# Kernel tuning notes

Measured on AMD Instinct MI355X. Metric: run time of the kernel, lower is better.

## Reference

```python
import jax, jax.numpy as jnp
import numpy as np

NUM = 21  # classes 1..NUM scored; bin 0 is background, bin NUM+1 is a dump bin


def _class_counts(y_pred, y_true):
    # Single-pass histogram over all classes instead of O(num) full-tensor scans.
    yp = y_pred.ravel()
    yt = y_true.ravel()
    nbins = NUM + 2
    cnt_true = jnp.zeros((nbins,), jnp.float32).at[yt].add(1.0)
    cnt_pred = jnp.zeros((nbins,), jnp.float32).at[yp].add(1.0)
    # intersection: positions where pred == true, binned by label; mismatches -> dump bin
    inter_idx = jnp.where(yp == yt, yt, NUM + 1)
    inter = jnp.zeros((nbins,), jnp.float32).at[inter_idx].add(1.0)
    return cnt_true, cnt_pred, inter


def setup_inputs() -> dict:
    key = jax.random.key(0)
    k1, k2 = jax.random.split(key)
    shape = (32, 1024, 1024)
    y_pred = jax.random.randint(k1, shape, 0, NUM + 1, dtype=jnp.int32)
    y_true = jax.random.randint(k2, shape, 0, NUM + 1, dtype=jnp.int32)
    return {"y_pred": y_pred, "y_true": y_true}


def reference(y_pred, y_true):
    cnt_true, cnt_pred, inter = _class_counts(y_pred, y_true)
    # classes 1..NUM (label 0 skipped, as in the original loop over range(1, num+1))
    c_true = cnt_true[1:NUM + 1]
    c_pred = cnt_pred[1:NUM + 1]
    c_inter = inter[1:NUM + 1]
    union = c_true + c_pred - c_inter
    iou = (c_inter + 1e-6) / (union + 1e-6)  # [NUM]
    present = (c_true > 0).astype(jnp.float32)
    mIoU = jnp.sum(iou * present) / jnp.maximum(jnp.sum(present), 1.0)
    return mIoU, iou
```

## Files before the change

### kernel.cpp

```cpp
#include <hip/hip_runtime.h>


#define NUMC  21
#define NBINS 22
#define JBINS (NBINS * NBINS)
#define RSTR  485
#define NREP  4
#define GRID  2048
#define TPB   256

typedef int iv4 __attribute__((ext_vector_type(4)));

#define LDP(J) __builtin_nontemporal_load(yp4 + (J))
#define LDT(J) __builtin_nontemporal_load(yt4 + (J))
#define DS4(P, T)                                      \
    atomicAdd(&hh[(T).x * NBINS + (P).x], 1u);         \
    atomicAdd(&hh[(T).y * NBINS + (P).y], 1u);         \
    atomicAdd(&hh[(T).z * NBINS + (P).z], 1u);         \
    atomicAdd(&hh[(T).w * NBINS + (P).w], 1u);

__global__ void __launch_bounds__(256) hist_joint(
        const int* __restrict__ yp, const int* __restrict__ yt,
        unsigned int* __restrict__ partials, int n) {
    __shared__ unsigned int h[NREP * RSTR];
    for (int i = threadIdx.x; i < NREP * RSTR; i += TPB) h[i] = 0u;
    __syncthreads();

    const int lane = threadIdx.x & 63;
    const int wave = threadIdx.x >> 6;
    unsigned int* hh = h + wave * RSTR;

    const iv4* __restrict__ yp4 = (const iv4*)yp;
    const iv4* __restrict__ yt4 = (const iv4*)yt;
    const int n4 = n >> 2;

    const int gwave   = blockIdx.x * 4 + wave;
    const int nwaves  = GRID * 4;
    const int wstride = nwaves * 128;
    const int sweeps  = n4 / wstride;

    if (sweeps * wstride == n4 && (n & 3) == 0) {
        const int j0 = gwave * 128 + lane;
        iv4 pa = LDP(j0),      pb = LDP(j0 + 64);
        iv4 ta = LDT(j0),      tb = LDT(j0 + 64);
        for (int it = 1; it < sweeps; ++it) {
            const int j = j0 + it * wstride;
            iv4 npa = LDP(j),      npb = LDP(j + 64);
            iv4 nta = LDT(j),      ntb = LDT(j + 64);
            DS4(pa, ta) DS4(pb, tb)
            pa = npa; pb = npb; ta = nta; tb = ntb;
        }
        DS4(pa, ta) DS4(pb, tb)
    } else {
        const int stride = GRID * TPB;
        const int i0 = blockIdx.x * TPB + threadIdx.x;
        if (i0 < n4) {
            iv4 p = LDP(i0), t = LDT(i0);
            for (int j = i0 + stride; j < n4; j += stride) {
                iv4 pn = LDP(j), tn = LDT(j);
                DS4(p, t)
                p = pn; t = tn;
            }
            DS4(p, t)
        }
        if (blockIdx.x == 0 && threadIdx.x == 0) {
            for (int k = n4 << 2; k < n; k++)
                atomicAdd(&hh[yt[k] * NBINS + yp[k]], 1u);
        }
    }
#undef DS4
#undef LDP
#undef LDT

    __syncthreads();
    for (int c = threadIdx.x; c < JBINS; c += TPB) {
        unsigned int s = h[c] + h[RSTR + c] + h[2 * RSTR + c] + h[3 * RSTR + c];
        partials[(size_t)blockIdx.x * JBINS + c] = s;
    }
}

__global__ void __launch_bounds__(256) reduce_partials(
        const unsigned int* __restrict__ partials,
        unsigned int* __restrict__ g, int nblocks) {
    __shared__ unsigned int lds[256];
    const int c = blockIdx.x;
    unsigned int s = 0;
    for (int b = threadIdx.x; b < nblocks; b += 256)
        s += partials[(size_t)b * JBINS + c];
    lds[threadIdx.x] = s;
    __syncthreads();
    for (int w = 128; w > 0; w >>= 1) {
        if (threadIdx.x < w) lds[threadIdx.x] += lds[threadIdx.x + w];
        __syncthreads();
    }
    if (threadIdx.x == 0) g[c] = lds[0];
}

__global__ void finalize_kernel(const unsigned int* __restrict__ g,
                                float* __restrict__ out) {
    int lane = threadIdx.x;
    float iou = 0.0f, pres = 0.0f;
    if (lane >= 1 && lane <= NUMC) {
        unsigned int ct = 0, cp = 0;
        #pragma unroll
        for (int k = 0; k < NBINS; k++) {
            ct += g[lane * NBINS + k];
            cp += g[k * NBINS + lane];
        }
        unsigned int ci = g[lane * NBINS + lane];
        float u = (float)ct + (float)cp - (float)ci;
        iou = ((float)ci + 1e-6f) / (u + 1e-6f);
        pres = (ct > 0u) ? 1.0f : 0.0f;
        out[lane] = iou;
    }
    float v = iou * pres, pc = pres;
    #pragma unroll
    for (int off = 32; off > 0; off >>= 1) {
        v += __shfl_down(v, off);
        pc += __shfl_down(pc, off);
    }
    if (lane == 0) out[0] = v / fmaxf(pc, 1.0f);
}

extern "C" void kernel_launch(void* const* d_in, const int* in_sizes, int n_in,
                              void* d_out, int out_size, void* d_ws, size_t ws_size,
                              hipStream_t stream) {
    const int* yp = (const int*)d_in[0];
    const int* yt = (const int*)d_in[1];
    int n = in_sizes[0];
    float* out = (float*)d_out;

    unsigned int* g = (unsigned int*)d_ws;
    unsigned int* partials = g + JBINS;

    hist_joint<<<GRID, TPB, 0, stream>>>(yp, yt, partials, n);
    reduce_partials<<<JBINS, 256, 0, stream>>>(partials, g, GRID);
    finalize_kernel<<<1, 64, 0, stream>>>(g, out);
}
```

Baseline: 258.4 us.

## Fuse partial reduction and finalize into one kernel using a last-block ticket

Replaces the per-bin reduction kernel and the separate finalize kernel with one kernel. In it, 128 blocks each sum 16 rows of partial histograms, add the sums atomically into a global histogram, and the last block to arrive (found via an atomic ticket) computes the IoU output. The global histogram and the ticket are zeroed by block 0 of the histogram kernel. This drops one kernel launch and gives coalesced row reads in place of strided column reads, at the cost of global atomics and a fence-based handoff.

```diff
diff --git a/kernel.cpp b/kernel.cpp
--- a/kernel.cpp
+++ b/kernel.cpp
@@ -8,6 +8,8 @@
 #define NREP  4
 #define GRID  2048
 #define TPB   256
+#define RBLK  128
+#define ROWS  (GRID / RBLK)
 
 typedef int iv4 __attribute__((ext_vector_type(4)));
 
@@ -21,7 +23,13 @@
 
 __global__ void __launch_bounds__(256) hist_joint(
         const int* __restrict__ yp, const int* __restrict__ yt,
-        unsigned int* __restrict__ partials, int n) {
+        unsigned int* __restrict__ partials,
+        unsigned int* __restrict__ gz,
+        int n) {
+    if (blockIdx.x == 0) {
+        for (int i = threadIdx.x; i < JBINS + 8; i += TPB) gz[i] = 0u;
+    }
+
     __shared__ unsigned int h[NREP * RSTR];
     for (int i = threadIdx.x; i < NREP * RSTR; i += TPB) h[i] = 0u;
     __syncthreads();
@@ -79,35 +87,50 @@
     }
 }
 
-__global__ void __launch_bounds__(256) reduce_partials(
+__global__ void __launch_bounds__(256) reduce_finalize(
         const unsigned int* __restrict__ partials,
-        unsigned int* __restrict__ g, int nblocks) {
-    __shared__ unsigned int lds[256];
-    const int c = blockIdx.x;
-    unsigned int s = 0;
-    for (int b = threadIdx.x; b < nblocks; b += 256)
-        s += partials[(size_t)b * JBINS + c];
-    lds[threadIdx.x] = s;
+        unsigned int* __restrict__ g,
+        unsigned int* __restrict__ ticket,
+        float* __restrict__ out) {
+    const int tid = threadIdx.x;
+
+    unsigned int s0 = 0u, s1 = 0u;
+    const unsigned int* base = partials + (size_t)blockIdx.x * ROWS * JBINS;
+    #pragma unroll 4
+    for (int r = 0; r < ROWS; ++r) {
+        const unsigned int* row = base + (size_t)r * JBINS;
+        s0 += row[tid];
+        if (tid < JBINS - 256) s1 += row[tid + 256];
+    }
+    atomicAdd(&g[tid], s0);
+    if (tid < JBINS - 256) atomicAdd(&g[tid + 256], s1);
+
+    __shared__ unsigned int islast;
     __syncthreads();
-    for (int w = 128; w > 0; w >>= 1) {
-        if (threadIdx.x < w) lds[threadIdx.x] += lds[threadIdx.x + w];
-        __syncthreads();
+    if (tid == 0) {
+        __threadfence();
+        unsigned int old = __hip_atomic_fetch_add(
+            ticket, 1u, __ATOMIC_ACQ_REL, __HIP_MEMORY_SCOPE_AGENT);
+        islast = (old == RBLK - 1) ? 1u : 0u;
     }
-    if (threadIdx.x == 0) g[c] = lds[0];
-}
+    __syncthreads();
+    if (!islast) return;
+    __threadfence();
 
-__global__ void finalize_kernel(const unsigned int* __restrict__ g,
-                                float* __restrict__ out) {
-    int lane = threadIdx.x;
+    const int lane = tid;
+    if (lane >= 64) return;
     float iou = 0.0f, pres = 0.0f;
     if (lane >= 1 && lane <= NUMC) {
-        unsigned int ct = 0, cp = 0;
+        unsigned int ct = 0u, cp = 0u;
         #pragma unroll
         for (int k = 0; k < NBINS; k++) {
-            ct += g[lane * NBINS + k];
-            cp += g[k * NBINS + lane];
+            ct += __hip_atomic_load(&g[lane * NBINS + k],
+                                    __ATOMIC_RELAXED, __HIP_MEMORY_SCOPE_AGENT);
+            cp += __hip_atomic_load(&g[k * NBINS + lane],
+                                    __ATOMIC_RELAXED, __HIP_MEMORY_SCOPE_AGENT);
         }
-        unsigned int ci = g[lane * NBINS + lane];
+        unsigned int ci = __hip_atomic_load(&g[lane * NBINS + lane],
+                                    __ATOMIC_RELAXED, __HIP_MEMORY_SCOPE_AGENT);
         float u = (float)ct + (float)cp - (float)ci;
         iou = ((float)ci + 1e-6f) / (u + 1e-6f);
         pres = (ct > 0u) ? 1.0f : 0.0f;
@@ -131,9 +154,9 @@
     float* out = (float*)d_out;
 
     unsigned int* g = (unsigned int*)d_ws;
-    unsigned int* partials = g + JBINS;
+    unsigned int* ticket = g + JBINS;
+    unsigned int* partials = g + JBINS + 8;
 
-    hist_joint<<<GRID, TPB, 0, stream>>>(yp, yt, partials, n);
-    reduce_partials<<<JBINS, 256, 0, stream>>>(partials, g, GRID);
-    finalize_kernel<<<1, 64, 0, stream>>>(g, out);
+    hist_joint<<<GRID, TPB, 0, stream>>>(yp, yt, partials, g, n);
+    reduce_finalize<<<RBLK, TPB, 0, stream>>>(partials, g, ticket, out);
 }
```

New measurement: 262.4 us. No clear change (+1.5%).
